# Optimization experiments

Hardware: AMD Instinct MI355X
Metric: run time of the kernel (lower is better)

The kernel has to match this reference:

```python
import jax, jax.numpy as jnp
import numpy as np

B, T, D, N, MW, WEMB = 1, 4096, 1024, 8192, 30, 20


def setup_inputs() -> dict:
    key = jax.random.key(0)
    k0, k1, k2, k3, k4 = jax.random.split(key, 5)
    inputs = jax.random.normal(k0, (B, T, D), dtype=jnp.float32)
    b = jax.random.randint(k1, (B, N), 0, T - MW)
    width = jax.random.randint(k2, (B, N), 0, MW)
    e = b + width  # e in [b, b+MW), always < T
    # learned params (std=0.02 init as in module)
    embed_w = (jax.random.normal(k3, (MW, WEMB), dtype=jnp.float32) * 0.02)
    attn_w = (jax.random.normal(k4, (D, 1), dtype=jnp.float32) * 0.02)
    attn_b = jnp.zeros((1,), dtype=jnp.float32)
    return {"inputs": inputs, "b": b, "e": e, "max_width": MW,
            "embed_w": embed_w, "attn_w": attn_w, "attn_b": attn_b}


def reference(inputs, b, e, max_width, embed_w, attn_w, attn_b):
    # inputs: [B,T,D], b/e: [B,N] int. Dropout is identity (eval mode).
    Bv, Tv, Dv = inputs.shape
    gather = jax.vmap(lambda x, idx: x[idx])  # [T,D],[N] -> [N,D]

    b_vec = gather(inputs, b)                                   # [B,N,D]
    e_vec = gather(inputs, jnp.minimum(e, Tv - 1))              # [B,N,D]

    width_idx = e - b                                           # [B,N]
    width_emb = embed_w[width_idx]                              # [B,N,WEMB]

    # attention-weighted head embedding (batch 0 only, as in original)
    token_attn = (inputs[0] @ attn_w)[:, 0] + attn_b[0]         # [T]
    tok = jnp.arange(Tv)
    span_mask = (tok[None, :] >= b[0][:, None]) & (tok[None, :] <= e[0][:, None])  # [N,T]
    # log(mask) + attn == where(mask, attn, -inf); each span has >=1 token
    attn = jax.nn.softmax(jnp.where(span_mask, token_attn[None, :], -jnp.inf), axis=1)
    head_emb = (attn @ inputs[0])[None]                         # [1,N,D]

    # masked span average
    w = jnp.arange(max_width)
    idxs = b[:, :, None] + w                                    # [B,N,W]
    span_toks = jax.vmap(lambda x, idx: x[idx])(inputs, jnp.minimum(idxs, Tv - 1))  # [B,N,W,D]
    m = (idxs <= e[:, :, None]).astype(inputs.dtype)            # [B,N,W]
    probs = m / m.sum(-1, keepdims=True)
    span_avg = jnp.einsum('bnw,bnwd->bnd', probs, span_toks)    # [B,N,D]

    vec = jnp.concatenate([b_vec, e_vec, width_emb, head_emb, span_avg], axis=-1)
    return vec, width_idx
```

## Files before the change

### kernel.cpp

```cpp
#include <hip/hip_runtime.h>
#include <math.h>

#define TT 4096
#define DD 1024
#define NSPAN 8192
#define MW 30
#define WEMB 20
#define VECW (4*DD + WEMB)

typedef float nf4 __attribute__((ext_vector_type(4)));

__global__ void __launch_bounds__(1024) prep_kernel(
        const float* __restrict__ x,
        const float* __restrict__ attn_w,
        const float* __restrict__ attn_b,
        const int* __restrict__ bptr,
        float* __restrict__ ta,
        int* __restrict__ perm) {
    const int tid = threadIdx.x;
    if (blockIdx.x == 0) {
        __shared__ int h[TT];
        __shared__ int wsum[16];
        #pragma unroll
        for (int k = 0; k < 4; ++k) h[tid * 4 + k] = 0;
        __syncthreads();
        #pragma unroll
        for (int k = 0; k < NSPAN / 1024; ++k)
            atomicAdd(&h[bptr[k * 1024 + tid]], 1);
        __syncthreads();
        const int v0 = h[tid*4+0], v1 = h[tid*4+1], v2 = h[tid*4+2], v3 = h[tid*4+3];
        const int s = v0 + v1 + v2 + v3;
        const int lane = tid & 63;
        int incl = s;
        #pragma unroll
        for (int off = 1; off < 64; off <<= 1) {
            int t = __shfl_up(incl, off);
            if (lane >= off) incl += t;
        }
        if (lane == 63) wsum[tid >> 6] = incl;
        __syncthreads();
        if (tid < 16) {
            int ws = wsum[tid];
            #pragma unroll
            for (int off = 1; off < 16; off <<= 1) {
                int t = __shfl_up(ws, off);
                if (tid >= off) ws += t;
            }
            wsum[tid] = ws;
        }
        __syncthreads();
        const int waveoff = (tid >> 6) == 0 ? 0 : wsum[(tid >> 6) - 1];
        int excl = waveoff + (incl - s);
        h[tid*4+0] = excl;  excl += v0;
        h[tid*4+1] = excl;  excl += v1;
        h[tid*4+2] = excl;  excl += v2;
        h[tid*4+3] = excl;
        __syncthreads();
        #pragma unroll
        for (int k = 0; k < NSPAN / 1024; ++k) {
            const int n = k * 1024 + tid;
            const int pos = atomicAdd(&h[bptr[n]], 1);
            perm[pos] = n;
        }
    } else {
        const int sub = tid >> 8;
        const int l   = tid & 255;
        const int t   = (blockIdx.x - 1) * 4 + sub;
        const float4 v = ((const float4*)(x + (size_t)t * DD))[l];
        const float4 w = ((const float4*)attn_w)[l];
        float s = v.x * w.x + v.y * w.y + v.z * w.z + v.w * w.w;
        #pragma unroll
        for (int off = 32; off > 0; off >>= 1) s += __shfl_down(s, off);
        __shared__ float part[16];
        if ((tid & 63) == 0) part[tid >> 6] = s;
        __syncthreads();
        if (l == 0)
            ta[t] = part[sub*4] + part[sub*4+1] + part[sub*4+2] + part[sub*4+3]
                  + attn_b[0];
    }
}

__global__ void span_kernel(const float* __restrict__ x,
                            const int* __restrict__ bptr,
                            const int* __restrict__ eptr,
                            const float* __restrict__ embed_w,
                            const float* __restrict__ ta,
                            const int* __restrict__ perm,
                            float* __restrict__ out) {
    const int spos = (blockIdx.x & 7) * (NSPAN / 8) + (blockIdx.x >> 3);
    const int n    = perm[spos];
    const int tid  = threadIdx.x;
    const int b     = bptr[n];
    const int e_raw = eptr[n];
    const int e     = min(e_raw, TT - 1);
    const int width = e_raw - b;
    const int len   = e - b + 1;

    __shared__ float wsm[32];
    if (tid < 64) {
        float v = (tid < len) ? ta[b + tid] : -INFINITY;
        float m = v;
        #pragma unroll
        for (int off = 32; off > 0; off >>= 1) m = fmaxf(m, __shfl_down(m, off));
        m = __shfl(m, 0);
        float ex = (tid < len) ? expf(v - m) : 0.0f;
        float s = ex;
        #pragma unroll
        for (int off = 32; off > 0; off >>= 1) s += __shfl_down(s, off);
        s = __shfl(s, 0);
        if (tid < len) wsm[tid] = ex / s;
    }
    __syncthreads();

    float* orow = out + (size_t)n * VECW;
    const float4* xrow = (const float4*)(x + (size_t)b * DD);

    float4 v = xrow[tid];
    {
        nf4 nv = { v.x, v.y, v.z, v.w };
        __builtin_nontemporal_store(nv, (nf4*)(orow) + tid);
    }
    float w0 = wsm[0];
    float4 acc_h = make_float4(w0 * v.x, w0 * v.y, w0 * v.z, w0 * v.w);
    float4 acc_a = v;
    for (int i = 1; i < len; ++i) {
        const float4 nv = xrow[(size_t)i * 256 + tid];
        const float w = wsm[i];
        acc_h.x += w * nv.x; acc_h.y += w * nv.y; acc_h.z += w * nv.z; acc_h.w += w * nv.w;
        acc_a.x += nv.x;     acc_a.y += nv.y;     acc_a.z += nv.z;     acc_a.w += nv.w;
        v = nv;
    }
    {
        nf4 nv = { v.x, v.y, v.z, v.w };
        __builtin_nontemporal_store(nv, (nf4*)(orow + DD) + tid);
    }
    const float inv = 1.0f / (float)len;
    acc_a.x *= inv; acc_a.y *= inv; acc_a.z *= inv; acc_a.w *= inv;
    nf4 nh = { acc_h.x, acc_h.y, acc_h.z, acc_h.w };
    nf4 na = { acc_a.x, acc_a.y, acc_a.z, acc_a.w };
    __builtin_nontemporal_store(nh, (nf4*)(orow + 2*DD + WEMB) + tid);
    __builtin_nontemporal_store(na, (nf4*)(orow + 3*DD + WEMB) + tid);

    if (tid < WEMB)
        __builtin_nontemporal_store(embed_w[width * WEMB + tid], orow + 2*DD + tid);
    if (tid == 0)
        __builtin_nontemporal_store((float)width, out + (size_t)NSPAN * VECW + n);
}

extern "C" void kernel_launch(void* const* d_in, const int* in_sizes, int n_in,
                              void* d_out, int out_size, void* d_ws, size_t ws_size,
                              hipStream_t stream) {
    const float* x       = (const float*)d_in[0];
    const int*   b       = (const int*)  d_in[1];
    const int*   e       = (const int*)  d_in[2];
    const float* embed_w = (const float*)d_in[4];
    const float* attn_w  = (const float*)d_in[5];
    const float* attn_b  = (const float*)d_in[6];
    float* out = (float*)d_out;

    float* ta   = (float*)d_ws;
    int*   perm = (int*)(ta + TT);

    prep_kernel<<<1 + TT/4, 1024, 0, stream>>>(x, attn_w, attn_b, b, ta, perm);
    span_kernel<<<NSPAN, 256, 0, stream>>>(x, b, e, embed_w, ta, perm, out);
}
```

Baseline: 48.73 us.

## Fuse token attention dot into span kernel with one wave per span

```diff
diff --git a/kernel.cpp b/kernel.cpp
--- a/kernel.cpp
+++ b/kernel.cpp
@@ -10,140 +10,158 @@
 
 typedef float nf4 __attribute__((ext_vector_type(4)));
 
-__global__ void __launch_bounds__(1024) prep_kernel(
-        const float* __restrict__ x,
-        const float* __restrict__ attn_w,
-        const float* __restrict__ attn_b,
-        const int* __restrict__ bptr,
-        float* __restrict__ ta,
-        int* __restrict__ perm) {
+static __device__ __forceinline__ float dot4(const float4 a, const float4 b) {
+    return fmaf(a.w, b.w, fmaf(a.z, b.z, fmaf(a.y, b.y, a.x * b.x)));
+}
+static __device__ __forceinline__ void fma4(float4& acc, const float w, const float4 v) {
+    acc.x = fmaf(w, v.x, acc.x); acc.y = fmaf(w, v.y, acc.y);
+    acc.z = fmaf(w, v.z, acc.z); acc.w = fmaf(w, v.w, acc.w);
+}
+static __device__ __forceinline__ void add4(float4& acc, const float4 v) {
+    acc.x += v.x; acc.y += v.y; acc.z += v.z; acc.w += v.w;
+}
+static __device__ __forceinline__ void nstore(const float4 v, float* p) {
+    nf4 t = { v.x, v.y, v.z, v.w };
+    __builtin_nontemporal_store(t, (nf4*)p);
+}
+
+__global__ void __launch_bounds__(1024) sort_kernel(const int* __restrict__ bptr,
+                                                    int* __restrict__ perm) {
     const int tid = threadIdx.x;
-    if (blockIdx.x == 0) {
-        __shared__ int h[TT];
-        __shared__ int wsum[16];
+    __shared__ int h[TT];
+    __shared__ int wsum[16];
+    #pragma unroll
+    for (int k = 0; k < 4; ++k) h[tid * 4 + k] = 0;
+    __syncthreads();
+    #pragma unroll
+    for (int k = 0; k < NSPAN / 1024; ++k)
+        atomicAdd(&h[bptr[k * 1024 + tid]], 1);
+    __syncthreads();
+    const int v0 = h[tid*4+0], v1 = h[tid*4+1], v2 = h[tid*4+2], v3 = h[tid*4+3];
+    const int s = v0 + v1 + v2 + v3;
+    const int lane = tid & 63;
+    int incl = s;
+    #pragma unroll
+    for (int off = 1; off < 64; off <<= 1) {
+        int t = __shfl_up(incl, off);
+        if (lane >= off) incl += t;
+    }
+    if (lane == 63) wsum[tid >> 6] = incl;
+    __syncthreads();
+    if (tid < 16) {
+        int ws = wsum[tid];
         #pragma unroll
-        for (int k = 0; k < 4; ++k) h[tid * 4 + k] = 0;
-        __syncthreads();
-        #pragma unroll
-        for (int k = 0; k < NSPAN / 1024; ++k)
-            atomicAdd(&h[bptr[k * 1024 + tid]], 1);
-        __syncthreads();
-        const int v0 = h[tid*4+0], v1 = h[tid*4+1], v2 = h[tid*4+2], v3 = h[tid*4+3];
-        const int s = v0 + v1 + v2 + v3;
-        const int lane = tid & 63;
-        int incl = s;
-        #pragma unroll
-        for (int off = 1; off < 64; off <<= 1) {
-            int t = __shfl_up(incl, off);
-            if (lane >= off) incl += t;
+        for (int off = 1; off < 16; off <<= 1) {
+            int t = __shfl_up(ws, off);
+            if (tid >= off) ws += t;
         }
-        if (lane == 63) wsum[tid >> 6] = incl;
-        __syncthreads();
-        if (tid < 16) {
-            int ws = wsum[tid];
-            #pragma unroll
-            for (int off = 1; off < 16; off <<= 1) {
-                int t = __shfl_up(ws, off);
-                if (tid >= off) ws += t;
-            }
-            wsum[tid] = ws;
-        }
-        __syncthreads();
-        const int waveoff = (tid >> 6) == 0 ? 0 : wsum[(tid >> 6) - 1];
-        int excl = waveoff + (incl - s);
-        h[tid*4+0] = excl;  excl += v0;
-        h[tid*4+1] = excl;  excl += v1;
-        h[tid*4+2] = excl;  excl += v2;
-        h[tid*4+3] = excl;
-        __syncthreads();
-        #pragma unroll
-        for (int k = 0; k < NSPAN / 1024; ++k) {
-            const int n = k * 1024 + tid;
-            const int pos = atomicAdd(&h[bptr[n]], 1);
-            perm[pos] = n;
-        }
-    } else {
-        const int sub = tid >> 8;
-        const int l   = tid & 255;
-        const int t   = (blockIdx.x - 1) * 4 + sub;
-        const float4 v = ((const float4*)(x + (size_t)t * DD))[l];
-        const float4 w = ((const float4*)attn_w)[l];
-        float s = v.x * w.x + v.y * w.y + v.z * w.z + v.w * w.w;
-        #pragma unroll
-        for (int off = 32; off > 0; off >>= 1) s += __shfl_down(s, off);
-        __shared__ float part[16];
-        if ((tid & 63) == 0) part[tid >> 6] = s;
-        __syncthreads();
-        if (l == 0)
-            ta[t] = part[sub*4] + part[sub*4+1] + part[sub*4+2] + part[sub*4+3]
-                  + attn_b[0];
+        wsum[tid] = ws;
+    }
+    __syncthreads();
+    const int waveoff = (tid >> 6) == 0 ? 0 : wsum[(tid >> 6) - 1];
+    int excl = waveoff + (incl - s);
+    h[tid*4+0] = excl;  excl += v0;
+    h[tid*4+1] = excl;  excl += v1;
+    h[tid*4+2] = excl;  excl += v2;
+    h[tid*4+3] = excl;
+    __syncthreads();
+    #pragma unroll
+    for (int k = 0; k < NSPAN / 1024; ++k) {
+        const int n = k * 1024 + tid;
+        const int pos = atomicAdd(&h[bptr[n]], 1);
+        perm[pos] = n;
     }
 }
 
-__global__ void span_kernel(const float* __restrict__ x,
-                            const int* __restrict__ bptr,
-                            const int* __restrict__ eptr,
-                            const float* __restrict__ embed_w,
-                            const float* __restrict__ ta,
-                            const int* __restrict__ perm,
-                            float* __restrict__ out) {
-    const int spos = (blockIdx.x & 7) * (NSPAN / 8) + (blockIdx.x >> 3);
+#define PROC_ROW(C0, C1, C2, C3) do {                                        \
+        float pd = (dot4(C0, w0) + dot4(C1, w1))                             \
+                 + (dot4(C2, w2) + dot4(C3, w3));                            \
+        pd += __shfl_xor(pd, 32); pd += __shfl_xor(pd, 16);                  \
+        pd += __shfl_xor(pd, 8);  pd += __shfl_xor(pd, 4);                   \
+        pd += __shfl_xor(pd, 2);  pd += __shfl_xor(pd, 1);                   \
+        const float wg = exp2f(pd * 1.44269504f);                            \
+        ssum += wg;                                                          \
+        fma4(h0, wg, C0); fma4(h1, wg, C1); fma4(h2, wg, C2); fma4(h3, wg, C3); \
+        add4(a0, C0); add4(a1, C1); add4(a2, C2); add4(a3, C3);              \
+    } while (0)
+
+__global__ void __launch_bounds__(256, 4) span_kernel(
+        const float* __restrict__ x,
+        const int* __restrict__ bptr,
+        const int* __restrict__ eptr,
+        const float* __restrict__ embed_w,
+        const float* __restrict__ attn_w,
+        const int* __restrict__ perm,
+        float* __restrict__ out) {
+    const int tid = threadIdx.x;
+    const int wv  = tid >> 6;
+    const int l   = tid & 63;
+    const int blk  = (blockIdx.x & 7) * (NSPAN / 4 / 8) + (blockIdx.x >> 3);
+    const int spos = blk * 4 + wv;
     const int n    = perm[spos];
-    const int tid  = threadIdx.x;
     const int b     = bptr[n];
     const int e_raw = eptr[n];
     const int e     = min(e_raw, TT - 1);
     const int width = e_raw - b;
     const int len   = e - b + 1;
 
-    __shared__ float wsm[32];
-    if (tid < 64) {
-        float v = (tid < len) ? ta[b + tid] : -INFINITY;
-        float m = v;
-        #pragma unroll
-        for (int off = 32; off > 0; off >>= 1) m = fmaxf(m, __shfl_down(m, off));
-        m = __shfl(m, 0);
-        float ex = (tid < len) ? expf(v - m) : 0.0f;
-        float s = ex;
-        #pragma unroll
-        for (int off = 32; off > 0; off >>= 1) s += __shfl_down(s, off);
-        s = __shfl(s, 0);
-        if (tid < len) wsm[tid] = ex / s;
+    const float4* aw = (const float4*)attn_w;
+    const float4 w0 = aw[l], w1 = aw[64 + l], w2 = aw[128 + l], w3 = aw[192 + l];
+
+    const float4* xr = (const float4*)(x + (size_t)b * DD);
+    float* orow = out + (size_t)n * VECW;
+
+    float4 c0 = xr[l], c1 = xr[64 + l], c2 = xr[128 + l], c3 = xr[192 + l];
+    nstore(c0, orow + 4*l);
+    nstore(c1, orow + 4*(64 + l));
+    nstore(c2, orow + 4*(128 + l));
+    nstore(c3, orow + 4*(192 + l));
+
+    float  ssum = 0.0f;
+    float4 h0 = {0,0,0,0}, h1 = {0,0,0,0}, h2 = {0,0,0,0}, h3 = {0,0,0,0};
+    float4 a0 = {0,0,0,0}, a1 = {0,0,0,0}, a2 = {0,0,0,0}, a3 = {0,0,0,0};
+
+    for (int i = 1; i < len; ++i) {
+        const float4* row = xr + (size_t)i * 256;
+        const float4 n0 = row[l], n1 = row[64 + l], n2 = row[128 + l], n3 = row[192 + l];
+        PROC_ROW(c0, c1, c2, c3);
+        c0 = n0; c1 = n1; c2 = n2; c3 = n3;
     }
-    __syncthreads();
+    PROC_ROW(c0, c1, c2, c3);
 
-    float* orow = out + (size_t)n * VECW;
-    const float4* xrow = (const float4*)(x + (size_t)b * DD);
+    float* esec = orow + DD;
+    nstore(c0, esec + 4*l);
+    nstore(c1, esec + 4*(64 + l));
+    nstore(c2, esec + 4*(128 + l));
+    nstore(c3, esec + 4*(192 + l));
 
-    float4 v = xrow[tid];
-    {
-        nf4 nv = { v.x, v.y, v.z, v.w };
-        __builtin_nontemporal_store(nv, (nf4*)(orow) + tid);
+    const float invs = 1.0f / ssum;
+    const float invl = 1.0f / (float)len;
+    h0.x *= invs; h0.y *= invs; h0.z *= invs; h0.w *= invs;
+    h1.x *= invs; h1.y *= invs; h1.z *= invs; h1.w *= invs;
+    h2.x *= invs; h2.y *= invs; h2.z *= invs; h2.w *= invs;
+    h3.x *= invs; h3.y *= invs; h3.z *= invs; h3.w *= invs;
+    a0.x *= invl; a0.y *= invl; a0.z *= invl; a0.w *= invl;
+    a1.x *= invl; a1.y *= invl; a1.z *= invl; a1.w *= invl;
+    a2.x *= invl; a2.y *= invl; a2.z *= invl; a2.w *= invl;
+    a3.x *= invl; a3.y *= invl; a3.z *= invl; a3.w *= invl;
+
+    float* hsec = orow + 2*DD + WEMB;
+    nstore(h0, hsec + 4*l);
+    nstore(h1, hsec + 4*(64 + l));
+    nstore(h2, hsec + 4*(128 + l));
+    nstore(h3, hsec + 4*(192 + l));
+    float* asec = orow + 3*DD + WEMB;
+    nstore(a0, asec + 4*l);
+    nstore(a1, asec + 4*(64 + l));
+    nstore(a2, asec + 4*(128 + l));
+    nstore(a3, asec + 4*(192 + l));
+
+    if (l < 5) {
+        const float4 we = ((const float4*)(embed_w + width * WEMB))[l];
+        nstore(we, orow + 2*DD + 4*l);
     }
-    float w0 = wsm[0];
-    float4 acc_h = make_float4(w0 * v.x, w0 * v.y, w0 * v.z, w0 * v.w);
-    float4 acc_a = v;
-    for (int i = 1; i < len; ++i) {
-        const float4 nv = xrow[(size_t)i * 256 + tid];
-        const float w = wsm[i];
-        acc_h.x += w * nv.x; acc_h.y += w * nv.y; acc_h.z += w * nv.z; acc_h.w += w * nv.w;
-        acc_a.x += nv.x;     acc_a.y += nv.y;     acc_a.z += nv.z;     acc_a.w += nv.w;
-        v = nv;
-    }
-    {
-        nf4 nv = { v.x, v.y, v.z, v.w };
-        __builtin_nontemporal_store(nv, (nf4*)(orow + DD) + tid);
-    }
-    const float inv = 1.0f / (float)len;
-    acc_a.x *= inv; acc_a.y *= inv; acc_a.z *= inv; acc_a.w *= inv;
-    nf4 nh = { acc_h.x, acc_h.y, acc_h.z, acc_h.w };
-    nf4 na = { acc_a.x, acc_a.y, acc_a.z, acc_a.w };
-    __builtin_nontemporal_store(nh, (nf4*)(orow + 2*DD + WEMB) + tid);
-    __builtin_nontemporal_store(na, (nf4*)(orow + 3*DD + WEMB) + tid);
-
-    if (tid < WEMB)
-        __builtin_nontemporal_store(embed_w[width * WEMB + tid], orow + 2*DD + tid);
-    if (tid == 0)
+    if (l == 63)
         __builtin_nontemporal_store((float)width, out + (size_t)NSPAN * VECW + n);
 }
 
@@ -155,12 +173,10 @@
     const int*   e       = (const int*)  d_in[2];
     const float* embed_w = (const float*)d_in[4];
     const float* attn_w  = (const float*)d_in[5];
-    const float* attn_b  = (const float*)d_in[6];
     float* out = (float*)d_out;
 
-    float* ta   = (float*)d_ws;
-    int*   perm = (int*)(ta + TT);
+    int* perm = (int*)d_ws;
 
-    prep_kernel<<<1 + TT/4, 1024, 0, stream>>>(x, attn_w, attn_b, b, ta, perm);
-    span_kernel<<<NSPAN, 256, 0, stream>>>(x, b, e, embed_w, ta, perm, out);
+    sort_kernel<<<1, 1024, 0, stream>>>(b, perm);
+    span_kernel<<<NSPAN / 4, 256, 0, stream>>>(x, b, e, embed_w, attn_w, perm, out);
 }
```

Result: slower. 52.28 us (+7.3%).

## Compute span softmax per wave with shuffles and drop shared-memory barrier

Applied to the files above, without the earlier changes.

```diff
diff --git a/kernel.cpp b/kernel.cpp
--- a/kernel.cpp
+++ b/kernel.cpp
@@ -9,6 +9,14 @@
 #define VECW (4*DD + WEMB)
 
 typedef float nf4 __attribute__((ext_vector_type(4)));
+
+static __device__ __forceinline__ float dot4(const float4 a, const float4 b) {
+    return fmaf(a.w, b.w, fmaf(a.z, b.z, fmaf(a.y, b.y, a.x * b.x)));
+}
+static __device__ __forceinline__ void nstore(const float4 v, float* p) {
+    nf4 t = { v.x, v.y, v.z, v.w };
+    __builtin_nontemporal_store(t, (nf4*)p);
+}
 
 __global__ void __launch_bounds__(1024) prep_kernel(
         const float* __restrict__ x,
@@ -63,86 +71,76 @@
             perm[pos] = n;
         }
     } else {
-        const int sub = tid >> 8;
-        const int l   = tid & 255;
-        const int t   = (blockIdx.x - 1) * 4 + sub;
-        const float4 v = ((const float4*)(x + (size_t)t * DD))[l];
-        const float4 w = ((const float4*)attn_w)[l];
-        float s = v.x * w.x + v.y * w.y + v.z * w.z + v.w * w.w;
-        #pragma unroll
-        for (int off = 32; off > 0; off >>= 1) s += __shfl_down(s, off);
-        __shared__ float part[16];
-        if ((tid & 63) == 0) part[tid >> 6] = s;
-        __syncthreads();
-        if (l == 0)
-            ta[t] = part[sub*4] + part[sub*4+1] + part[sub*4+2] + part[sub*4+3]
-                  + attn_b[0];
+        const int wv = tid >> 6;
+        const int l  = tid & 63;
+        const int t  = (blockIdx.x - 1) * 16 + wv;
+        const float4* xr = (const float4*)(x + (size_t)t * DD);
+        const float4* aw = (const float4*)attn_w;
+        const float4 v0 = xr[l], v1 = xr[64 + l], v2 = xr[128 + l], v3 = xr[192 + l];
+        const float4 w0 = aw[l], w1 = aw[64 + l], w2 = aw[128 + l], w3 = aw[192 + l];
+        float s = (dot4(v0, w0) + dot4(v1, w1)) + (dot4(v2, w2) + dot4(v3, w3));
+        s += __shfl_xor(s, 32); s += __shfl_xor(s, 16);
+        s += __shfl_xor(s, 8);  s += __shfl_xor(s, 4);
+        s += __shfl_xor(s, 2);  s += __shfl_xor(s, 1);
+        if (l == 0) ta[t] = s + attn_b[0];
     }
 }
 
-__global__ void span_kernel(const float* __restrict__ x,
-                            const int* __restrict__ bptr,
-                            const int* __restrict__ eptr,
-                            const float* __restrict__ embed_w,
-                            const float* __restrict__ ta,
-                            const int* __restrict__ perm,
-                            float* __restrict__ out) {
+__global__ void __launch_bounds__(256, 8) span_kernel(
+        const float* __restrict__ x,
+        const int* __restrict__ bptr,
+        const int* __restrict__ eptr,
+        const float* __restrict__ embed_w,
+        const float* __restrict__ ta,
+        const int* __restrict__ perm,
+        float* __restrict__ out) {
+    const int tid = threadIdx.x;
+    const int l   = tid & 63;
     const int spos = (blockIdx.x & 7) * (NSPAN / 8) + (blockIdx.x >> 3);
     const int n    = perm[spos];
-    const int tid  = threadIdx.x;
     const int b     = bptr[n];
     const int e_raw = eptr[n];
     const int e     = min(e_raw, TT - 1);
     const int width = e_raw - b;
     const int len   = e - b + 1;
 
-    __shared__ float wsm[32];
-    if (tid < 64) {
-        float v = (tid < len) ? ta[b + tid] : -INFINITY;
-        float m = v;
-        #pragma unroll
-        for (int off = 32; off > 0; off >>= 1) m = fmaxf(m, __shfl_down(m, off));
-        m = __shfl(m, 0);
-        float ex = (tid < len) ? expf(v - m) : 0.0f;
-        float s = ex;
-        #pragma unroll
-        for (int off = 32; off > 0; off >>= 1) s += __shfl_down(s, off);
-        s = __shfl(s, 0);
-        if (tid < len) wsm[tid] = ex / s;
-    }
-    __syncthreads();
-
+    const float4* xrow = (const float4*)(x + (size_t)b * DD);
     float* orow = out + (size_t)n * VECW;
-    const float4* xrow = (const float4*)(x + (size_t)b * DD);
 
     float4 v = xrow[tid];
-    {
-        nf4 nv = { v.x, v.y, v.z, v.w };
-        __builtin_nontemporal_store(nv, (nf4*)(orow) + tid);
-    }
-    float w0 = wsm[0];
+
+    float ex = (l < len) ? exp2f(ta[b + l] * 1.44269504f) : 0.0f;
+    float ssum = ex;
+    ssum += __shfl_xor(ssum, 32); ssum += __shfl_xor(ssum, 16);
+    ssum += __shfl_xor(ssum, 8);  ssum += __shfl_xor(ssum, 4);
+    ssum += __shfl_xor(ssum, 2);  ssum += __shfl_xor(ssum, 1);
+
+    nstore(v, orow + 4*tid);
+
+    const float w0 = __shfl(ex, 0);
     float4 acc_h = make_float4(w0 * v.x, w0 * v.y, w0 * v.z, w0 * v.w);
     float4 acc_a = v;
     for (int i = 1; i < len; ++i) {
         const float4 nv = xrow[(size_t)i * 256 + tid];
-        const float w = wsm[i];
-        acc_h.x += w * nv.x; acc_h.y += w * nv.y; acc_h.z += w * nv.z; acc_h.w += w * nv.w;
-        acc_a.x += nv.x;     acc_a.y += nv.y;     acc_a.z += nv.z;     acc_a.w += nv.w;
+        const float w = __shfl(ex, i);
+        acc_h.x = fmaf(w, nv.x, acc_h.x); acc_h.y = fmaf(w, nv.y, acc_h.y);
+        acc_h.z = fmaf(w, nv.z, acc_h.z); acc_h.w = fmaf(w, nv.w, acc_h.w);
+        acc_a.x += nv.x; acc_a.y += nv.y; acc_a.z += nv.z; acc_a.w += nv.w;
         v = nv;
     }
-    {
-        nf4 nv = { v.x, v.y, v.z, v.w };
-        __builtin_nontemporal_store(nv, (nf4*)(orow + DD) + tid);
+    nstore(v, orow + DD + 4*tid);
+
+    const float invs = 1.0f / ssum;
+    const float invl = 1.0f / (float)len;
+    acc_h.x *= invs; acc_h.y *= invs; acc_h.z *= invs; acc_h.w *= invs;
+    acc_a.x *= invl; acc_a.y *= invl; acc_a.z *= invl; acc_a.w *= invl;
+    nstore(acc_h, orow + 2*DD + WEMB + 4*tid);
+    nstore(acc_a, orow + 3*DD + WEMB + 4*tid);
+
+    if (tid < 5) {
+        const float4 we = ((const float4*)(embed_w + width * WEMB))[tid];
+        nstore(we, orow + 2*DD + 4*tid);
     }
-    const float inv = 1.0f / (float)len;
-    acc_a.x *= inv; acc_a.y *= inv; acc_a.z *= inv; acc_a.w *= inv;
-    nf4 nh = { acc_h.x, acc_h.y, acc_h.z, acc_h.w };
-    nf4 na = { acc_a.x, acc_a.y, acc_a.z, acc_a.w };
-    __builtin_nontemporal_store(nh, (nf4*)(orow + 2*DD + WEMB) + tid);
-    __builtin_nontemporal_store(na, (nf4*)(orow + 3*DD + WEMB) + tid);
-
-    if (tid < WEMB)
-        __builtin_nontemporal_store(embed_w[width * WEMB + tid], orow + 2*DD + tid);
     if (tid == 0)
         __builtin_nontemporal_store((float)width, out + (size_t)NSPAN * VECW + n);
 }
@@ -161,6 +159,6 @@
     float* ta   = (float*)d_ws;
     int*   perm = (int*)(ta + TT);
 
-    prep_kernel<<<1 + TT/4, 1024, 0, stream>>>(x, attn_w, attn_b, b, ta, perm);
+    prep_kernel<<<1 + TT/16, 1024, 0, stream>>>(x, attn_w, attn_b, b, ta, perm);
     span_kernel<<<NSPAN, 256, 0, stream>>>(x, b, e, embed_w, ta, perm, out);
 }
```

New measurement: 52.47 us. 1.08x slower.
